# Kernel tuning notes

Measured on AMD Instinct MI355X. Metric: run time of the kernel, lower is better.

Reference implementation:

```python
import jax, jax.numpy as jnp
import numpy as np
from jax import lax

DIM = 512


def rmsnorm(x, gamma):
    # F.normalize(x, dim=-1) * sqrt(dim) * (gamma + 1)
    n = jnp.maximum(jnp.linalg.norm(x, axis=-1, keepdims=True), 1e-12)
    return x / n * (DIM ** 0.5) * (gamma + 1.0)


def lru_layer(x, Wn, Wif, Whf, bhf):
    # x: [b, t, d]. Precompute the input-dependent projections as big matmuls,
    # then scan the genuinely sequential hidden recurrence.
    nh = jnp.tanh(jnp.einsum('btd,de->bte', x, Wn))   # candidate hidden
    ifg = jnp.einsum('btd,de->bte', x, Wif)            # input forget logits
    b = x.shape[0]
    h0 = jnp.zeros((b, DIM), dtype=x.dtype)            # init_hidden buffer (zeros)

    def step(h, inp):
        nh_t, if_t = inp                               # [b, d] each
        g = jax.nn.sigmoid(h @ Whf + bhf + if_t)       # forget gate
        h_next = h + g * (nh_t - h)                    # lerp(h, nh, g)
        return h_next, h_next

    _, hs = lax.scan(step, h0, (jnp.swapaxes(nh, 0, 1), jnp.swapaxes(ifg, 0, 1)))
    return jnp.swapaxes(hs, 0, 1)                      # [b, t, d]


def gate_cell(x, hidden, Wn, Wif, Whf, bhf):
    # LightRecurrentUnitCell applied pointwise over [b, t, d] with hidden=x_in
    nh = jnp.tanh(jnp.einsum('btd,de->bte', x, Wn))
    g = jax.nn.sigmoid(jnp.einsum('btd,de->bte', hidden, Whf) + bhf
                       + jnp.einsum('btd,de->bte', x, Wif))
    return hidden + g * (nh - hidden)


def setup_inputs() -> dict:
    key = jax.random.key(0)
    ks = jax.random.split(key, 12)
    s = 1.0 / np.sqrt(DIM)
    def w(k):
        return jax.random.uniform(k, (DIM, DIM), jnp.float32, -s, s)
    inp = {
        'x': jax.random.normal(ks[0], (32, 2048, DIM), jnp.float32),
        'gamma': jnp.zeros((DIM,), jnp.float32),
        'g_Wn': w(ks[1]), 'g_Wif': w(ks[2]), 'g_Whf': w(ks[3]),
        'g_bhf': jax.random.uniform(ks[4], (DIM,), jnp.float32, -s, s),
        'l0_Wn': w(ks[5]), 'l0_Wif': w(ks[6]), 'l0_Whf': w(ks[7]),
        'l0_bhf': jax.random.uniform(ks[8], (DIM,), jnp.float32, -s, s),
        'l1_Wn': w(ks[9]), 'l1_Wif': w(ks[10]), 'l1_Whf': w(ks[11]),
        'l1_bhf': jax.random.uniform(jax.random.fold_in(key, 99), (DIM,), jnp.float32, -s, s),
    }
    return inp


def reference(x, gamma, g_Wn, g_Wif, g_Whf, g_bhf,
              l0_Wn, l0_Wif, l0_Whf, l0_bhf,
              l1_Wn, l1_Wif, l1_Whf, l1_bhf):
    xn = rmsnorm(x, gamma)
    h = lru_layer(xn, l0_Wn, l0_Wif, l0_Whf, l0_bhf)
    h = lru_layer(h, l1_Wn, l1_Wif, l1_Whf, l1_bhf)
    lru_out = gate_cell(h, xn, g_Wn, g_Wif, g_Whf, g_bhf)
    return lru_out + x
```

## Files before the change

kernel.cpp:

```cpp
#include <hip/hip_runtime.h>
#include <stdint.h>

#define D 512
#define BATCH 32
#define TT 2048
#define BT (BATCH*TT)

typedef unsigned short u16;
typedef __attribute__((ext_vector_type(8))) short bf16x8;
typedef __attribute__((ext_vector_type(4))) float f32x4;

__device__ __forceinline__ float bf2f(u16 u){
  union { unsigned int i; float f; } v; v.i = ((unsigned int)u) << 16; return v.f;
}
__device__ __forceinline__ u16 f2bf(float f){
  union { float f; unsigned int i; } v; v.f = f;
  unsigned int r = (v.i + 0x7fffu + ((v.i >> 16) & 1u)) >> 16;
  return (u16)r;
}

__device__ __forceinline__ int dot4i8(int a, int b, int c){
#if __has_builtin(__builtin_amdgcn_sdot4)
  return __builtin_amdgcn_sdot4(a, b, c, false);
#else
  c += (int)(char)(a      ) * (int)(char)(b      );
  c += (int)(char)(a >>  8) * (int)(char)(b >>  8);
  c += (int)(char)(a >> 16) * (int)(char)(b >> 16);
  c += (int)(char)(a >> 24) * (int)(char)(b >> 24);
  return c;
#endif
}

__global__ __launch_bounds__(256) void rmsnorm_k(const float* __restrict__ x,
                                                 const float* __restrict__ gamma,
                                                 u16* __restrict__ xn){
  int row = blockIdx.x;
  int t = threadIdx.x;
  const float* xr = x + (size_t)row * D;
  float v0 = xr[t];
  float v1 = xr[t + 256];
  float s = v0*v0 + v1*v1;
  #pragma unroll
  for (int o = 32; o > 0; o >>= 1) s += __shfl_down(s, o);
  __shared__ float red[4];
  int lane = t & 63, wv = t >> 6;
  if (lane == 0) red[wv] = s;
  __syncthreads();
  float tot = red[0] + red[1] + red[2] + red[3];
  float n = fmaxf(sqrtf(tot), 1e-12f);
  float sc = 22.627416997969522f / n;
  u16* o_ = xn + (size_t)row * D;
  o_[t]       = f2bf(v0 * sc * (gamma[t] + 1.f));
  o_[t + 256] = f2bf(v1 * sc * (gamma[t + 256] + 1.f));
}

__global__ __launch_bounds__(256) void transpose_k(const float* __restrict__ src,
                                                   u16* __restrict__ dst){
  __shared__ u16 tile[32][33];
  int bx = blockIdx.x * 32, by = blockIdx.y * 32;
  int tx = threadIdx.x & 31, ty = threadIdx.x >> 5;
  #pragma unroll
  for (int i = 0; i < 32; i += 8)
    tile[ty + i][tx] = f2bf(src[(size_t)(by + ty + i) * D + bx + tx]);
  __syncthreads();
  #pragma unroll
  for (int i = 0; i < 32; i += 8)
    dst[(size_t)(bx + ty + i) * D + by + tx] = tile[tx][ty + i];
}

__global__ __launch_bounds__(64) void quant_col_k(const float* __restrict__ W,
                                                  int* __restrict__ Wq,
                                                  float* __restrict__ sc){
  int e = blockIdx.x;
  int lane = threadIdx.x;
  float w[8];
  float m = 0.f;
  #pragma unroll
  for (int j = 0; j < 8; j++){
    w[j] = W[(size_t)(lane*8 + j) * D + e];
    m = fmaxf(m, fabsf(w[j]));
  }
  #pragma unroll
  for (int o = 32; o > 0; o >>= 1) m = fmaxf(m, __shfl_xor(m, o));
  float inv = (m > 0.f) ? (127.f / m) : 0.f;
  int q[8];
  #pragma unroll
  for (int j = 0; j < 8; j++){
    int v = __float2int_rn(w[j] * inv);
    v = v < -127 ? -127 : (v > 127 ? 127 : v);
    q[j] = v & 0xff;
  }
  int p0 = q[0] | (q[1] << 8) | (q[2] << 16) | (q[3] << 24);
  int p1 = q[4] | (q[5] << 8) | (q[6] << 16) | (q[7] << 24);
  Wq[e*128 + lane*2]     = p0;
  Wq[e*128 + lane*2 + 1] = p1;
  if (lane == 0) sc[e] = m / (127.f * 127.f);
}

__global__ __launch_bounds__(256) void gemm_bt_k(const u16* __restrict__ A,
                                                 const u16* __restrict__ Bt,
                                                 u16* __restrict__ C,
                                                 int do_tanh){
  __shared__ __align__(16) u16 As[128*32];
  __shared__ __align__(16) u16 Bs[128*32];
  int tid = threadIdx.x;
  int bm = blockIdx.x, bn = blockIdx.y;
  int wv = tid >> 6, lane = tid & 63;
  int wm = (wv & 1) * 64, wn = (wv >> 1) * 64;
  int m0 = lane & 15, quad = lane >> 4;
  f32x4 acc[4][4];
  #pragma unroll
  for (int i = 0; i < 4; i++)
    #pragma unroll
    for (int j = 0; j < 4; j++){
      f32x4 z = {0.f, 0.f, 0.f, 0.f};
      acc[i][j] = z;
    }
  const size_t arow = (size_t)bm * 128;
  const size_t brow = (size_t)bn * 128;
  for (int k0 = 0; k0 < D; k0 += 32){
    __syncthreads();
    #pragma unroll
    for (int i = 0; i < 2; i++){
      int c = tid + 256*i;
      int r = c >> 2, ko = (c & 3) * 8;
      ((int4*)As)[c] = *(const int4*)(A  + (arow + r) * D + k0 + ko);
      ((int4*)Bs)[c] = *(const int4*)(Bt + (brow + r) * D + k0 + ko);
    }
    __syncthreads();
    bf16x8 af[4], bfr[4];
    #pragma unroll
    for (int i = 0; i < 4; i++){
      af[i]  = *(const bf16x8*)(As + (wm + i*16 + m0) * 32 + quad*8);
      bfr[i] = *(const bf16x8*)(Bs + (wn + i*16 + m0) * 32 + quad*8);
    }
    #pragma unroll
    for (int i = 0; i < 4; i++)
      #pragma unroll
      for (int j = 0; j < 4; j++)
        acc[i][j] = __builtin_amdgcn_mfma_f32_16x16x32_bf16(af[i], bfr[j], acc[i][j], 0, 0, 0);
  }
  #pragma unroll
  for (int i = 0; i < 4; i++)
    #pragma unroll
    for (int j = 0; j < 4; j++)
      #pragma unroll
      for (int r = 0; r < 4; r++){
        size_t row = arow + wm + i*16 + quad*4 + r;
        int col = bn*128 + wn + j*16 + m0;
        float v = acc[i][j][r];
        if (do_tanh) v = tanhf(v);
        C[row * D + col] = f2bf(v);
      }
}

__global__ __launch_bounds__(512, 2) void lru_scan_k(u16* __restrict__ Nn,
                                                     const u16* __restrict__ Ff,
                                                     const int* __restrict__ Wq,
                                                     const float* __restrict__ sc,
                                                     const float* __restrict__ bhf){
  int e = threadIdx.x;
  int b = blockIdx.x;
  int w[128];
  #pragma unroll
  for (int i = 0; i < 128; i++) w[i] = Wq[e*128 + i];
  float scale = sc[e];
  float bias  = bhf[e];
  __shared__ __align__(16) int hq[2][128];
  if (e < 128) hq[0][e] = 0;
  float h = 0.f;
  const size_t base = (size_t)b * TT * D + e;
  u16* np = Nn + base;
  const u16* fp = Ff + base;
  float nv = bf2f(np[0]);
  float fv = bf2f(fp[0]);
  __syncthreads();
  for (int t = 0; t < TT; t++){
    float nv_n = 0.f, fv_n = 0.f;
    if (t < TT - 1){
      nv_n = bf2f(np[(size_t)(t+1) * D]);
      fv_n = bf2f(fp[(size_t)(t+1) * D]);
    }
    const int* hb = hq[t & 1];
    int z = 0;
    #pragma unroll
    for (int i = 0; i < 32; i++){
      int4 hc = ((const int4*)hb)[i];
      z = dot4i8(w[4*i+0], hc.x, z);
      z = dot4i8(w[4*i+1], hc.y, z);
      z = dot4i8(w[4*i+2], hc.z, z);
      z = dot4i8(w[4*i+3], hc.w, z);
    }
    float arg = (float)z * scale + bias + fv;
    float g = 1.f / (1.f + __expf(-arg));
    h = h + g * (nv - h);
    np[(size_t)t * D] = f2bf(h);
    int q = __float2int_rn(h * 127.f);
    q = q < -127 ? -127 : (q > 127 ? 127 : q);
    ((char*)hq[(t+1) & 1])[e] = (char)q;
    nv = nv_n; fv = fv_n;
    __syncthreads();
  }
}

__global__ __launch_bounds__(256) void final1_k(const u16* __restrict__ xn,
                                                u16* __restrict__ Nng,
                                                const u16* __restrict__ Ffg,
                                                const u16* __restrict__ Ghf,
                                                const float* __restrict__ gbhf){
  size_t i = (size_t)blockIdx.x * 256 + threadIdx.x;
  int e = (int)(i & (D - 1));
  float xnv = bf2f(xn[i]);
  float nv  = bf2f(Nng[i]);
  float arg = bf2f(Ghf[i]) + gbhf[e] + bf2f(Ffg[i]);
  float g = 1.f / (1.f + __expf(-arg));
  float lru = xnv + g * (nv - xnv);
  Nng[i] = f2bf(lru);
}

__global__ __launch_bounds__(256) void final2_k(const u16* __restrict__ lru,
                                                const float* __restrict__ x,
                                                float* __restrict__ out){
  size_t i = (size_t)blockIdx.x * 256 + threadIdx.x;
  out[i] = bf2f(lru[i]) + x[i];
}

extern "C" void kernel_launch(void* const* d_in, const int* in_sizes, int n_in,
                              void* d_out, int out_size, void* d_ws, size_t ws_size,
                              hipStream_t stream){
  const float* x      = (const float*)d_in[0];
  const float* gamma  = (const float*)d_in[1];
  const float* g_Wn   = (const float*)d_in[2];
  const float* g_Wif  = (const float*)d_in[3];
  const float* g_Whf  = (const float*)d_in[4];
  const float* g_bhf  = (const float*)d_in[5];
  const float* l0_Wn  = (const float*)d_in[6];
  const float* l0_Wif = (const float*)d_in[7];
  const float* l0_Whf = (const float*)d_in[8];
  const float* l0_bhf = (const float*)d_in[9];
  const float* l1_Wn  = (const float*)d_in[10];
  const float* l1_Wif = (const float*)d_in[11];
  const float* l1_Whf = (const float*)d_in[12];
  const float* l1_bhf = (const float*)d_in[13];
  float* out = (float*)d_out;

  char* ws = (char*)d_ws;
  const size_t PLANE = (size_t)BT * D * 2;
  u16* P0 = (u16*)(ws);
  u16* P1 = (u16*)(ws + PLANE);
  u16* P2 = (u16*)d_out;
  u16* P3 = P2 + (size_t)BT * D;

  char* wb = ws + 2*PLANE;
  const size_t WSZ = (size_t)D * D * 2;
  u16* T_l0Wn  = (u16*)(wb + 0*WSZ);
  u16* T_l0Wif = (u16*)(wb + 1*WSZ);
  u16* T_gWhf  = (u16*)(wb + 2*WSZ);
  u16* T_l1Wn  = (u16*)(wb + 3*WSZ);
  u16* T_l1Wif = (u16*)(wb + 4*WSZ);
  u16* T_gWn   = (u16*)(wb + 5*WSZ);
  u16* T_gWif  = (u16*)(wb + 6*WSZ);
  int*   Wq0 = (int*)  (wb + 7*WSZ);
  int*   Wq1 = (int*)  (wb + 7*WSZ + (size_t)D*D);
  float* sc0 = (float*)(wb + 7*WSZ + 2*(size_t)D*D);
  float* sc1 = (float*)(wb + 7*WSZ + 2*(size_t)D*D + D*4);

  dim3 tb(256), tg(16, 16);
  transpose_k<<<tg, tb, 0, stream>>>(l0_Wn,  T_l0Wn);
  transpose_k<<<tg, tb, 0, stream>>>(l0_Wif, T_l0Wif);
  transpose_k<<<tg, tb, 0, stream>>>(g_Whf,  T_gWhf);
  transpose_k<<<tg, tb, 0, stream>>>(l1_Wn,  T_l1Wn);
  transpose_k<<<tg, tb, 0, stream>>>(l1_Wif, T_l1Wif);
  transpose_k<<<tg, tb, 0, stream>>>(g_Wn,   T_gWn);
  transpose_k<<<tg, tb, 0, stream>>>(g_Wif,  T_gWif);
  quant_col_k<<<512, 64, 0, stream>>>(l0_Whf, Wq0, sc0);
  quant_col_k<<<512, 64, 0, stream>>>(l1_Whf, Wq1, sc1);

  rmsnorm_k<<<BT, 256, 0, stream>>>(x, gamma, P0);

  dim3 gg(BT/128, D/128);
  gemm_bt_k<<<gg, tb, 0, stream>>>(P0, T_l0Wn,  P1, 1);
  gemm_bt_k<<<gg, tb, 0, stream>>>(P0, T_l0Wif, P2, 0);
  lru_scan_k<<<BATCH, 512, 0, stream>>>(P1, P2, Wq0, sc0, l0_bhf);
  gemm_bt_k<<<gg, tb, 0, stream>>>(P1, T_l1Wn,  P3, 1);
  gemm_bt_k<<<gg, tb, 0, stream>>>(P1, T_l1Wif, P2, 0);
  lru_scan_k<<<BATCH, 512, 0, stream>>>(P3, P2, Wq1, sc1, l1_bhf);
  gemm_bt_k<<<gg, tb, 0, stream>>>(P3, T_gWn,  P1, 1);
  gemm_bt_k<<<gg, tb, 0, stream>>>(P3, T_gWif, P2, 0);
  gemm_bt_k<<<gg, tb, 0, stream>>>(P0, T_gWhf, P3, 0);

  final1_k<<<BT*D/256, 256, 0, stream>>>(P0, P1, P2, P3, g_bhf);
  final2_k<<<BT*D/256, 256, 0, stream>>>(P1, x, out);
}
```

Baseline: 4.242 ms.

## Split scan matvec across lane groups with shuffle reduction and padded LDS

Restructures the recurrent int8 matvec in the scan kernel so each lane computes partial dot products for four output columns over a quarter of the K dimension, then reduces with cross-lane shuffles. The hidden-state buffer in shared memory is padded to cut bank conflicts, input prefetch is deepened to two steps ahead, and __syncthreads is replaced by a raw LDS waitcnt plus s_barrier. The goal is to shorten the per-step critical path (fewer serial dot4 ops per thread, more ILP) at the cost of shuffle overhead and more complex indexing.

```diff
diff --git a/kernel.cpp b/kernel.cpp
--- a/kernel.cpp
+++ b/kernel.cpp
@@ -159,47 +159,93 @@
                                                      const int* __restrict__ Wq,
                                                      const float* __restrict__ sc,
                                                      const float* __restrict__ bhf){
-  int e = threadIdx.x;
-  int b = blockIdx.x;
-  int w[128];
-  #pragma unroll
-  for (int i = 0; i < 128; i++) w[i] = Wq[e*128 + i];
-  float scale = sc[e];
-  float bias  = bhf[e];
-  __shared__ __align__(16) int hq[2][128];
-  if (e < 128) hq[0][e] = 0;
-  float h = 0.f;
-  const size_t base = (size_t)b * TT * D + e;
+  const int tid = threadIdx.x;
+  const int b   = blockIdx.x;
+  const int wv  = tid >> 6;
+  const int l   = tid & 63;
+  const int o   = l & 15;
+  const int gq  = l >> 4;
+  const int c0  = wv*64 + o*4;
+  const int c   = c0 + gq;
+
+  int w[4][32];
+  #pragma unroll
+  for (int j = 0; j < 4; j++){
+    const int4* src = (const int4*)(Wq + (c0 + j)*128 + gq*32);
+    #pragma unroll
+    for (int i = 0; i < 8; i++){
+      int4 v = src[i];
+      w[j][4*i+0] = v.x; w[j][4*i+1] = v.y; w[j][4*i+2] = v.z; w[j][4*i+3] = v.w;
+    }
+  }
+  const float scale = sc[c];
+  const float bias  = bhf[c];
+
+  __shared__ __align__(16) int hq[2][144];
+  for (int i = tid; i < 288; i += 512) ((int*)hq)[i] = 0;
+
+  const size_t base = (size_t)b * TT * D + c;
   u16* np = Nn + base;
   const u16* fp = Ff + base;
-  float nv = bf2f(np[0]);
-  float fv = bf2f(fp[0]);
+  float nv0 = bf2f(np[0]);
+  float fv0 = bf2f(fp[0]);
+  float nv1 = bf2f(np[D]);
+  float fv1 = bf2f(fp[D]);
+  float h = 0.f;
+
+  const int rbase = gq * 36;
+  const int wgrp  = c >> 7;
+  const int waddr = wgrp*144 + (c & 127);
+
   __syncthreads();
+
   for (int t = 0; t < TT; t++){
-    float nv_n = 0.f, fv_n = 0.f;
-    if (t < TT - 1){
-      nv_n = bf2f(np[(size_t)(t+1) * D]);
-      fv_n = bf2f(fp[(size_t)(t+1) * D]);
-    }
-    const int* hb = hq[t & 1];
-    int z = 0;
-    #pragma unroll
-    for (int i = 0; i < 32; i++){
+    int tp = t + 2; if (tp > TT-1) tp = TT-1;
+    float nvN = bf2f(np[(size_t)tp * D]);
+    float fvN = bf2f(fp[(size_t)tp * D]);
+
+    const int* hb = hq[t & 1] + rbase;
+    int z0 = 0, z1 = 0, z2 = 0, z3 = 0;
+    #pragma unroll
+    for (int i = 0; i < 8; i++){
       int4 hc = ((const int4*)hb)[i];
-      z = dot4i8(w[4*i+0], hc.x, z);
-      z = dot4i8(w[4*i+1], hc.y, z);
-      z = dot4i8(w[4*i+2], hc.z, z);
-      z = dot4i8(w[4*i+3], hc.w, z);
-    }
-    float arg = (float)z * scale + bias + fv;
+      z0 = dot4i8(w[0][4*i+0], hc.x, z0);
+      z1 = dot4i8(w[1][4*i+0], hc.x, z1);
+      z2 = dot4i8(w[2][4*i+0], hc.x, z2);
+      z3 = dot4i8(w[3][4*i+0], hc.x, z3);
+      z0 = dot4i8(w[0][4*i+1], hc.y, z0);
+      z1 = dot4i8(w[1][4*i+1], hc.y, z1);
+      z2 = dot4i8(w[2][4*i+1], hc.y, z2);
+      z3 = dot4i8(w[3][4*i+1], hc.y, z3);
+      z0 = dot4i8(w[0][4*i+2], hc.z, z0);
+      z1 = dot4i8(w[1][4*i+2], hc.z, z1);
+      z2 = dot4i8(w[2][4*i+2], hc.z, z2);
+      z3 = dot4i8(w[3][4*i+2], hc.z, z3);
+      z0 = dot4i8(w[0][4*i+3], hc.w, z0);
+      z1 = dot4i8(w[1][4*i+3], hc.w, z1);
+      z2 = dot4i8(w[2][4*i+3], hc.w, z2);
+      z3 = dot4i8(w[3][4*i+3], hc.w, z3);
+    }
+    z0 += __shfl_xor(z0, 16); z0 += __shfl_xor(z0, 32);
+    z1 += __shfl_xor(z1, 16); z1 += __shfl_xor(z1, 32);
+    z2 += __shfl_xor(z2, 16); z2 += __shfl_xor(z2, 32);
+    z3 += __shfl_xor(z3, 16); z3 += __shfl_xor(z3, 32);
+    int z = (gq == 0) ? z0 : (gq == 1) ? z1 : (gq == 2) ? z2 : z3;
+
+    float arg = (float)z * scale + bias + fv0;
     float g = 1.f / (1.f + __expf(-arg));
-    h = h + g * (nv - h);
+    h = h + g * (nv0 - h);
     np[(size_t)t * D] = f2bf(h);
     int q = __float2int_rn(h * 127.f);
     q = q < -127 ? -127 : (q > 127 ? 127 : q);
-    ((char*)hq[(t+1) & 1])[e] = (char)q;
-    nv = nv_n; fv = fv_n;
-    __syncthreads();
+    ((char*)hq[(t+1) & 1])[waddr] = (char)q;
+
+    nv0 = nv1; fv0 = fv1; nv1 = nvN; fv1 = fvN;
+
+    asm volatile("" ::: "memory");
+    __builtin_amdgcn_s_waitcnt(0xc07f);
+    __builtin_amdgcn_s_barrier();
+    asm volatile("" ::: "memory");
   }
 }
 
```

Result: slower. 4.680 ms (+10.3%).
